# Optimization experiments

Measured on AMD Instinct MI355X. Metric: run time of the kernel, lower is better.

Reference implementation:

```python
import jax, jax.numpy as jnp
import numpy as np

DIM = 1024
NUM_HEADS = 16
HEAD_DIM = DIM // NUM_HEADS  # 64
WINDOW = 256
SCALE = HEAD_DIM ** -0.5


def setup_inputs() -> dict:
    key = jax.random.key(0)
    ks = jax.random.split(key, 5)
    B, L = 4, 4096
    x = jax.random.normal(ks[0], (B, L, DIM), dtype=jnp.float32)
    # Linear weights stored torch-style as (out_features, in_features)
    q_w = jax.random.normal(ks[1], (DIM, DIM), dtype=jnp.float32) * (DIM ** -0.5)
    kv_w = jax.random.normal(ks[2], (2 * HEAD_DIM, DIM), dtype=jnp.float32) * (DIM ** -0.5)
    proj_w = jax.random.normal(ks[3], (DIM, DIM), dtype=jnp.float32) * (DIM ** -0.5)
    proj_b = jax.random.normal(ks[4], (DIM,), dtype=jnp.float32) * 0.01
    return {"x": x, "q_w": q_w, "kv_w": kv_w, "proj_w": proj_w, "proj_b": proj_b}


def reference(x, q_w, kv_w, proj_w, proj_b):
    B, L, D = x.shape
    H, hd, ws = NUM_HEADS, HEAD_DIM, WINDOW
    # MQA projections
    q = x @ q_w.T                                  # (B, L, D)
    kv = x @ kv_w.T                                # (B, L, 2*hd)
    k, v = kv[..., :hd], kv[..., hd:]              # (B, L, hd) single KV head
    q = q.reshape(B, L, H, hd).transpose(0, 2, 1, 3)  # (B, H, L, hd)
    # Pad sequence to a multiple of the window size (static at trace time)
    pad = (ws - L % ws) % ws
    Lp = L + pad
    if pad > 0:
        q = jnp.pad(q, ((0, 0), (0, 0), (0, pad), (0, 0)))
        k = jnp.pad(k, ((0, 0), (0, pad), (0, 0)))
        v = jnp.pad(v, ((0, 0), (0, pad), (0, 0)))
    n = Lp // ws
    qb = q.reshape(B, H, n, ws, hd)                # (B, H, n, w, d)
    kb = k.reshape(B, n, ws, hd)                   # (B, n, w, d) broadcast over heads
    vb = v.reshape(B, n, ws, hd)
    # Dense per-window attention with MQA-aware KV broadcast (no expand)
    attn = jnp.einsum('bhnwd,bnud->bhnwu', qb, kb) * SCALE
    attn = jax.nn.softmax(attn, axis=-1)
    out = jnp.einsum('bhnwu,bnud->bhnwd', attn, vb)  # (B, H, n, w, d)
    out = out.reshape(B, H, Lp, hd)[:, :, :L, :]
    out = out.transpose(0, 2, 1, 3).reshape(B, L, D)  # b h l d -> b l (h d)
    return out @ proj_w.T + proj_b
```

## Files before the change

kernel.cpp:

```cpp
#include <hip/hip_runtime.h>

typedef short bf16x8 __attribute__((ext_vector_type(8)));
typedef float f32x4 __attribute__((ext_vector_type(4)));

#define QSCALE 0.18033688011112042f

__device__ __forceinline__ unsigned short f2bf(float x) {
  unsigned int u = __float_as_uint(x);
  u = (u + 0x7FFFu + ((u >> 16) & 1u)) >> 16;
  return (unsigned short)u;
}

__device__ __forceinline__ unsigned pack_rn(float a, float b) {
  unsigned au = __float_as_uint(a) + 0x8000u;
  unsigned bu = __float_as_uint(b) + 0x8000u;
  return (bu & 0xFFFF0000u) | (au >> 16);
}

__device__ __forceinline__ void async16(const void* g, void* l) {
  typedef const __attribute__((address_space(1))) unsigned int* gp_t;
  typedef __attribute__((address_space(3))) unsigned int* lp_t;
  __builtin_amdgcn_global_load_lds((gp_t)g, (lp_t)l, 16, 0, 0);
}

union frag_u { bf16x8 f; unsigned int u[4]; };

__global__ void cast_bf16(const float* __restrict__ in, unsigned short* __restrict__ out, int n4) {
  int i = blockIdx.x * 256 + threadIdx.x;
  if (i >= n4) return;
  float4 v = ((const float4*)in)[i];
  ushort4 o;
  o.x = f2bf(v.x); o.y = f2bf(v.y); o.z = f2bf(v.z); o.w = f2bf(v.w);
  ((ushort4*)out)[i] = o;
}

__global__ void cast_w3(const float* __restrict__ qw, const float* __restrict__ kvw,
                        const float* __restrict__ pw, unsigned short* __restrict__ qwo,
                        unsigned short* __restrict__ kvwo, unsigned short* __restrict__ pwo) {
  int i = blockIdx.x * 256 + threadIdx.x;
  const float* src; unsigned short* dst; int j;
  if (i < 262144)      { src = qw;  dst = qwo;  j = i; }
  else if (i < 294912) { src = kvw; dst = kvwo; j = i - 262144; }
  else                 { src = pw;  dst = pwo;  j = i - 294912; }
  float4 v = ((const float4*)src)[j];
  ushort4 o;
  o.x = f2bf(v.x); o.y = f2bf(v.y); o.z = f2bf(v.z); o.w = f2bf(v.w);
  ((ushort4*)dst)[j] = o;
}

template<int MODE>
__global__ __launch_bounds__(512, 2) void gemm256(
    const unsigned short* __restrict__ A,
    const unsigned short* __restrict__ Bw,
    unsigned short* __restrict__ Cbf,
    float* __restrict__ Cf,
    const float* __restrict__ bias,
    const float oscale,
    int M, int N, int K)
{
  __shared__ unsigned short S[65536];
  const int t = threadIdx.x;
  const int lane = t & 63, wave = t >> 6;
  const int g = lane >> 4, r = lane & 15;
  const int wm = wave >> 2, wn = wave & 3;

  const int nby = N >> 8;
  const int cpx = gridDim.x >> 3;
  const int bid = blockIdx.x;
  const int swz = (bid & 7) * cpx + (bid >> 3);
  const long row0 = (long)(swz / nby) * 256;
  const long col0 = (long)(swz % nby) * 256;

  const int NT = K >> 6;

  auto stage = [&](const unsigned short* gsrc, long grow0, int kcol0, int region) {
#pragma unroll
    for (int i = 0; i < 2; ++i) {
      int o = (i * 512 + t) << 4;
      int row = o >> 7;
      int scol = (o & 127) ^ ((row & 7) << 4);
      async16(gsrc + (grow0 + row) * K + kcol0 + (scol >> 1),
              (char*)S + region + i * 8192 + wave * 1024);
    }
  };
  auto ldA = [&](int bo, int ar, int ks) {
    return *(const bf16x8*)((const char*)S + bo + ar * 128 +
                            ((ks * 64 + g * 16) ^ ((ar & 7) << 4)));
  };
  auto ldB = [&](int bo, int br, int ks) {
    return *(const bf16x8*)((const char*)S + bo + 32768 + br * 128 +
                            ((ks * 64 + g * 16) ^ ((br & 7) << 4)));
  };

  f32x4 acc[8][4] = {};
  bf16x8 aF[4][2], b01[2][2], b23[2][2];

  stage(A,  row0,       0, 0);
  stage(A,  row0 + 128, 0, 16384);
  stage(Bw, col0,       0, 32768);
  stage(Bw, col0 + 128, 0, 32768 + 16384);
  if (NT > 1) {
    stage(Bw, col0,       64, 65536 + 32768);
    stage(Bw, col0 + 128, 64, 65536 + 32768 + 16384);
    asm volatile("s_waitcnt vmcnt(4)" ::: "memory");
  } else {
    asm volatile("s_waitcnt vmcnt(0)" ::: "memory");
  }
  __builtin_amdgcn_s_barrier();

  for (int kt = 0; kt < NT; ++kt) {
    const int bo = (kt & 1) << 16;
#pragma unroll
    for (int mf = 0; mf < 4; ++mf) {
      int ar = wm * 128 + mf * 16 + r;
      aF[mf][0] = ldA(bo, ar, 0); aF[mf][1] = ldA(bo, ar, 1);
    }
#pragma unroll
    for (int nf = 0; nf < 2; ++nf) {
      int br = wn * 64 + nf * 16 + r;
      b01[nf][0] = ldB(bo, br, 0); b01[nf][1] = ldB(bo, br, 1);
    }
    if (kt + 1 < NT) stage(A, row0, (kt + 1) * 64, bo ^ 65536);
    __builtin_amdgcn_s_barrier();
    __builtin_amdgcn_s_setprio(1);
#pragma unroll
    for (int mf = 0; mf < 4; ++mf)
#pragma unroll
      for (int nf = 0; nf < 2; ++nf) {
        acc[mf][nf] = __builtin_amdgcn_mfma_f32_16x16x32_bf16(aF[mf][0], b01[nf][0], acc[mf][nf], 0, 0, 0);
        acc[mf][nf] = __builtin_amdgcn_mfma_f32_16x16x32_bf16(aF[mf][1], b01[nf][1], acc[mf][nf], 0, 0, 0);
      }
    __builtin_amdgcn_s_setprio(0);
#pragma unroll
    for (int nf = 0; nf < 2; ++nf) {
      int br = wn * 64 + (nf + 2) * 16 + r;
      b23[nf][0] = ldB(bo, br, 0); b23[nf][1] = ldB(bo, br, 1);
    }
    if (kt + 1 < NT) stage(A, row0 + 128, (kt + 1) * 64, (bo ^ 65536) + 16384);
    __builtin_amdgcn_s_barrier();
    __builtin_amdgcn_s_setprio(1);
#pragma unroll
    for (int mf = 0; mf < 4; ++mf)
#pragma unroll
      for (int nf = 0; nf < 2; ++nf) {
        acc[mf][nf + 2] = __builtin_amdgcn_mfma_f32_16x16x32_bf16(aF[mf][0], b23[nf][0], acc[mf][nf + 2], 0, 0, 0);
        acc[mf][nf + 2] = __builtin_amdgcn_mfma_f32_16x16x32_bf16(aF[mf][1], b23[nf][1], acc[mf][nf + 2], 0, 0, 0);
      }
    __builtin_amdgcn_s_setprio(0);
#pragma unroll
    for (int mf = 0; mf < 4; ++mf) {
      int ar = wm * 128 + (mf + 4) * 16 + r;
      aF[mf][0] = ldA(bo, ar, 0); aF[mf][1] = ldA(bo, ar, 1);
    }
    if (kt + 2 < NT) stage(Bw, col0, (kt + 2) * 64, bo + 32768);
    __builtin_amdgcn_s_barrier();
    __builtin_amdgcn_s_setprio(1);
#pragma unroll
    for (int mf = 0; mf < 4; ++mf)
#pragma unroll
      for (int nf = 0; nf < 2; ++nf) {
        acc[mf + 4][nf + 2] = __builtin_amdgcn_mfma_f32_16x16x32_bf16(aF[mf][0], b23[nf][0], acc[mf + 4][nf + 2], 0, 0, 0);
        acc[mf + 4][nf + 2] = __builtin_amdgcn_mfma_f32_16x16x32_bf16(aF[mf][1], b23[nf][1], acc[mf + 4][nf + 2], 0, 0, 0);
      }
    __builtin_amdgcn_s_setprio(0);
    if (kt + 2 < NT) stage(Bw, col0 + 128, (kt + 2) * 64, bo + 32768 + 16384);
    __builtin_amdgcn_s_setprio(1);
#pragma unroll
    for (int mf = 0; mf < 4; ++mf)
#pragma unroll
      for (int nf = 0; nf < 2; ++nf) {
        acc[mf + 4][nf] = __builtin_amdgcn_mfma_f32_16x16x32_bf16(aF[mf][0], b01[nf][0], acc[mf + 4][nf], 0, 0, 0);
        acc[mf + 4][nf] = __builtin_amdgcn_mfma_f32_16x16x32_bf16(aF[mf][1], b01[nf][1], acc[mf + 4][nf], 0, 0, 0);
      }
    __builtin_amdgcn_s_setprio(0);
    if (kt < NT - 2)      asm volatile("s_waitcnt vmcnt(4)" ::: "memory");
    else if (kt < NT - 1) asm volatile("s_waitcnt vmcnt(0)" ::: "memory");
    if (kt < NT - 1) __builtin_amdgcn_s_barrier();
  }

  if (MODE == 0) {
#pragma unroll
    for (int mf = 0; mf < 8; ++mf)
#pragma unroll
      for (int nf = 0; nf < 4; ++nf) {
        long rr = row0 + wm * 128 + mf * 16 + g * 4;
        long cc = col0 + wn * 64 + nf * 16 + r;
#pragma unroll
        for (int i = 0; i < 4; ++i)
          Cbf[(rr + i) * N + cc] = f2bf(acc[mf][nf][i] * oscale);
      }
  } else {
#pragma unroll
    for (int mf = 0; mf < 8; ++mf)
#pragma unroll
      for (int nf = 0; nf < 4; ++nf) {
        long rr = row0 + wm * 128 + mf * 16 + g * 4;
        long cc = col0 + wn * 64 + nf * 16 + r;
        float bb = bias[cc];
#pragma unroll
        for (int i = 0; i < 4; ++i)
          Cf[(rr + i) * N + cc] = acc[mf][nf][i] + bb;
      }
  }
}

__global__ __launch_bounds__(256) void gemm_kv(
    const unsigned short* __restrict__ A,
    const unsigned short* __restrict__ Bw,
    unsigned short* __restrict__ Kout,
    unsigned short* __restrict__ VTout,
    int M, int N, int K)
{
  __shared__ unsigned short As[128 * 64];
  __shared__ unsigned short Bs[128 * 64];
  const int t = threadIdx.x;
  const int lane = t & 63, wave = t >> 6;
  const int g = lane >> 4, r = lane & 15;
  const int wr = wave >> 1, wc = wave & 1;
  const long row0 = (long)blockIdx.x * 128;
  const long col0 = 0;

  f32x4 acc[4][4] = {};

  for (int kt = 0; kt < K; kt += 64) {
    __syncthreads();
#pragma unroll
    for (int i = 0; i < 4; ++i) {
      int o = (i * 256 + t) << 4;
      int arow = o >> 7;
      int scol = (o & 127) ^ ((arow & 7) << 4);
      async16(A + (row0 + arow) * K + kt + (scol >> 1), (char*)As + (i * 4096 + wave * 1024));
    }
#pragma unroll
    for (int i = 0; i < 4; ++i) {
      int o = (i * 256 + t) << 4;
      int brow = o >> 7;
      int scol = (o & 127) ^ ((brow & 7) << 4);
      async16(Bw + (col0 + brow) * K + kt + (scol >> 1), (char*)Bs + (i * 4096 + wave * 1024));
    }
    __syncthreads();
#pragma unroll
    for (int ks = 0; ks < 2; ++ks) {
      bf16x8 af[4], bfr[4];
#pragma unroll
      for (int rf = 0; rf < 4; ++rf) {
        int ar = wr * 64 + rf * 16 + r;
        af[rf] = *(const bf16x8*)((const char*)As + ar * 128 + ((ks * 64 + g * 16) ^ ((ar & 7) << 4)));
      }
#pragma unroll
      for (int cf = 0; cf < 4; ++cf) {
        int br = wc * 64 + cf * 16 + r;
        bfr[cf] = *(const bf16x8*)((const char*)Bs + br * 128 + ((ks * 64 + g * 16) ^ ((br & 7) << 4)));
      }
#pragma unroll
      for (int rf = 0; rf < 4; ++rf)
#pragma unroll
        for (int cf = 0; cf < 4; ++cf)
          acc[rf][cf] = __builtin_amdgcn_mfma_f32_16x16x32_bf16(af[rf], bfr[cf], acc[rf][cf], 0, 0, 0);
    }
  }

  if (wc == 0) {
#pragma unroll
    for (int rf = 0; rf < 4; ++rf)
#pragma unroll
      for (int cf = 0; cf < 4; ++cf) {
        long rr = row0 + wr * 64 + rf * 16 + g * 4;
        int cc = cf * 16 + r;
#pragma unroll
        for (int i = 0; i < 4; ++i)
          Kout[(rr + i) * 64 + cc] = f2bf(acc[rf][cf][i]);
      }
  } else {
#pragma unroll
    for (int rf = 0; rf < 4; ++rf)
#pragma unroll
      for (int cf = 0; cf < 4; ++cf) {
        long tok = row0 + wr * 64 + rf * 16 + g * 4;
        long w16 = tok >> 8;
        int kp = (int)(tok & 255);
        int hd = cf * 16 + r;
        ushort4 pk;
        pk.x = f2bf(acc[rf][cf][0]); pk.y = f2bf(acc[rf][cf][1]);
        pk.z = f2bf(acc[rf][cf][2]); pk.w = f2bf(acc[rf][cf][3]);
        *(ushort4*)(VTout + (w16 * 64 + hd) * 256 + kp) = pk;
      }
  }
}

__global__ __launch_bounds__(512, 2) void attn_win(
    const unsigned short* __restrict__ qb,
    const unsigned short* __restrict__ kb,
    const unsigned short* __restrict__ vt,
    unsigned short* __restrict__ ao)
{
  __shared__ unsigned short Ks[256 * 64];
  __shared__ unsigned short Vs[64 * 256];

  const int blk = blockIdx.x;
  const int hp = blk & 7;
  const int w16 = blk >> 3;
  const long tok0 = (long)w16 * 256;
  const int t = threadIdx.x;
  const int lane = t & 63, wave = t >> 6;
  const int g = lane >> 4, r = lane & 15;
  const int h = hp * 2 + (wave >> 2);
  const int qw = wave & 3;

#pragma unroll
  for (int i = 0; i < 4; ++i) {
    int o = (i * 512 + t) << 4;
    int row = o >> 7;
    int ph = ((row & 3) << 1) | ((row >> 3) & 1);
    int scol = (o & 127) ^ (ph << 4);
    async16(kb + (tok0 + row) * 64 + (scol >> 1), (char*)Ks + i * 8192 + wave * 1024);
  }
  const unsigned short* vbase = vt + (long)w16 * (64 * 256);
#pragma unroll
  for (int i = 0; i < 4; ++i) {
    int o = (i * 512 + t) << 4;
    int hd = o >> 9;
    int scol = (o & 511) ^ ((hd & 7) << 4);
    async16(vbase + (long)hd * 256 + (scol >> 1), (char*)Vs + i * 8192 + wave * 1024);
  }

  bf16x8 qf[4][2];
#pragma unroll
  for (int cq = 0; cq < 4; ++cq)
#pragma unroll
    for (int kh = 0; kh < 2; ++kh)
      qf[cq][kh] = *(const bf16x8*)(qb + (tok0 + qw * 64 + cq * 16 + r) * 1024 + h * 64 + kh * 32 + g * 8);

  f32x4 O[4][4] = {};
  float sp[4] = {0.f, 0.f, 0.f, 0.f};
  const int rsub = 8 * (r >> 2) + (r & 3);
  __syncthreads();

#pragma unroll
  for (int kc = 0; kc < 8; ++kc) {
    f32x4 sc[2][4] = {};
#pragma unroll
    for (int kr = 0; kr < 2; ++kr) {
      int kp = kc * 32 + kr * 4 + rsub;
      int ph = ((kp & 3) << 1) | ((kp >> 3) & 1);
      bf16x8 kf0 = *(const bf16x8*)((const char*)Ks + kp * 128 + ((g * 16) ^ (ph << 4)));
      bf16x8 kf1 = *(const bf16x8*)((const char*)Ks + kp * 128 + ((64 + g * 16) ^ (ph << 4)));
#pragma unroll
      for (int cq = 0; cq < 4; ++cq) {
        sc[kr][cq] = __builtin_amdgcn_mfma_f32_16x16x32_bf16(kf0, qf[cq][0], sc[kr][cq], 0, 0, 0);
        sc[kr][cq] = __builtin_amdgcn_mfma_f32_16x16x32_bf16(kf1, qf[cq][1], sc[kr][cq], 0, 0, 0);
      }
    }
    bf16x8 vf[4];
#pragma unroll
    for (int ch = 0; ch < 4; ++ch) {
      int hd = ch * 16 + r;
      vf[ch] = *(const bf16x8*)((const char*)Vs + hd * 512 + ((kc * 64 + g * 16) ^ ((hd & 7) << 4)));
    }
#pragma unroll
    for (int cq = 0; cq < 4; ++cq) {
#pragma unroll
      for (int kr = 0; kr < 2; ++kr)
#pragma unroll
        for (int i = 0; i < 4; ++i)
          sc[kr][cq][i] = __builtin_amdgcn_exp2f(sc[kr][cq][i]);
      sp[cq] += ((sc[0][cq][0] + sc[0][cq][1]) + (sc[0][cq][2] + sc[0][cq][3])) +
                ((sc[1][cq][0] + sc[1][cq][1]) + (sc[1][cq][2] + sc[1][cq][3]));
    }
#pragma unroll
    for (int rq = 0; rq < 4; ++rq) {
      frag_u pa;
      pa.u[0] = pack_rn(sc[0][rq][0], sc[0][rq][1]);
      pa.u[1] = pack_rn(sc[0][rq][2], sc[0][rq][3]);
      pa.u[2] = pack_rn(sc[1][rq][0], sc[1][rq][1]);
      pa.u[3] = pack_rn(sc[1][rq][2], sc[1][rq][3]);
#pragma unroll
      for (int ch = 0; ch < 4; ++ch)
        O[rq][ch] = __builtin_amdgcn_mfma_f32_16x16x32_bf16(pa.f, vf[ch], O[rq][ch], 0, 0, 0);
    }
  }
  float inv[4];
#pragma unroll
  for (int cq = 0; cq < 4; ++cq) {
    float s = sp[cq];
    s += __shfl_xor(s, 16);
    s += __shfl_xor(s, 32);
    inv[cq] = 1.0f / s;
  }
#pragma unroll
  for (int rq = 0; rq < 4; ++rq)
#pragma unroll
    for (int i = 0; i < 4; ++i) {
      float w = __shfl(inv[rq], g * 4 + i);
      long tokr = tok0 + qw * 64 + rq * 16 + g * 4 + i;
#pragma unroll
      for (int ch = 0; ch < 4; ++ch)
        ao[tokr * 1024 + h * 64 + ch * 16 + r] = f2bf(O[rq][ch][i] * w);
    }
}

extern "C" void kernel_launch(void* const* d_in, const int* in_sizes, int n_in,
                              void* d_out, int out_size, void* d_ws, size_t ws_size,
                              hipStream_t stream) {
  const float* x      = (const float*)d_in[0];
  const float* q_w    = (const float*)d_in[1];
  const float* kv_w   = (const float*)d_in[2];
  const float* proj_w = (const float*)d_in[3];
  const float* proj_b = (const float*)d_in[4];

  char* ws = (char*)d_ws;
  unsigned short* x_bf   = (unsigned short*)(ws + 0);
  unsigned short* q_bf   = (unsigned short*)(ws + 33554432);
  unsigned short* ao_bf  = (unsigned short*)(ws + 67108864);
  unsigned short* qw_bf  = (unsigned short*)(ws + 100663296);
  unsigned short* pw_bf  = (unsigned short*)(ws + 102760448);
  unsigned short* kvw_bf = (unsigned short*)(ws + 104857600);
  unsigned short* k_bf   = (unsigned short*)(ws + 105119744);
  unsigned short* vt_bf  = (unsigned short*)(ws + 107216896);
  if (ws_size < 109314048) return;

  cast_bf16<<<16384, 256, 0, stream>>>(x, x_bf, 4194304);
  cast_w3<<<2176, 256, 0, stream>>>(q_w, kv_w, proj_w, qw_bf, kvw_bf, pw_bf);

  gemm256<0><<<256, 512, 0, stream>>>(x_bf, qw_bf, q_bf, nullptr, nullptr, QSCALE, 16384, 1024, 1024);
  gemm_kv<<<128, 256, 0, stream>>>(x_bf, kvw_bf, k_bf, vt_bf, 16384, 128, 1024);
  attn_win<<<512, 512, 0, stream>>>(q_bf, k_bf, vt_bf, ao_bf);
  gemm256<1><<<256, 512, 0, stream>>>(ao_bf, pw_bf, nullptr, (float*)d_out, proj_b, 1.0f, 16384, 1024, 1024);
}
```

Baseline: 148.2 us.

## Fuse x fp32-to-bf16 cast into the KV projection GEMM

Removes the standalone cast_bf16 kernel and has the KV projection GEMM read x in fp32, convert it to bf16 in registers, write it to LDS for the MFMA, and also store the bf16 copy to global for the later Q GEMM. The KV GEMM now runs before the Q GEMM with 64-row tiles and 256 blocks, which saves one full read of x and one kernel launch. In exchange, the A-tile load becomes synchronous register loads instead of async LDS loads. Rounding also changes from round-to-nearest-even to pack_rn's simpler round-half-up, which alters bf16 values slightly.

```diff
diff --git a/kernel.cpp b/kernel.cpp
--- a/kernel.cpp
+++ b/kernel.cpp
@@ -2,6 +2,7 @@
 
 typedef short bf16x8 __attribute__((ext_vector_type(8)));
 typedef float f32x4 __attribute__((ext_vector_type(4)));
+typedef unsigned int u32x4 __attribute__((ext_vector_type(4)));
 
 #define QSCALE 0.18033688011112042f
 
@@ -24,15 +25,6 @@
 }
 
 union frag_u { bf16x8 f; unsigned int u[4]; };
-
-__global__ void cast_bf16(const float* __restrict__ in, unsigned short* __restrict__ out, int n4) {
-  int i = blockIdx.x * 256 + threadIdx.x;
-  if (i >= n4) return;
-  float4 v = ((const float4*)in)[i];
-  ushort4 o;
-  o.x = f2bf(v.x); o.y = f2bf(v.y); o.z = f2bf(v.z); o.w = f2bf(v.w);
-  ((ushort4*)out)[i] = o;
-}
 
 __global__ void cast_w3(const float* __restrict__ qw, const float* __restrict__ kvw,
                         const float* __restrict__ pw, unsigned short* __restrict__ qwo,
@@ -204,47 +196,57 @@
   }
 }
 
-__global__ __launch_bounds__(256) void gemm_kv(
-    const unsigned short* __restrict__ A,
+__global__ __launch_bounds__(256) void gemm_kv_cast(
+    const float* __restrict__ x,
     const unsigned short* __restrict__ Bw,
+    unsigned short* __restrict__ xbf,
     unsigned short* __restrict__ Kout,
-    unsigned short* __restrict__ VTout,
-    int M, int N, int K)
+    unsigned short* __restrict__ VTout)
 {
-  __shared__ unsigned short As[128 * 64];
+  __shared__ unsigned short As[64 * 64];
   __shared__ unsigned short Bs[128 * 64];
   const int t = threadIdx.x;
   const int lane = t & 63, wave = t >> 6;
   const int g = lane >> 4, r = lane & 15;
   const int wr = wave >> 1, wc = wave & 1;
-  const long row0 = (long)blockIdx.x * 128;
-  const long col0 = 0;
-
-  f32x4 acc[4][4] = {};
-
-  for (int kt = 0; kt < K; kt += 64) {
+  const long row0 = (long)blockIdx.x * 64;
+  const int arow = t >> 2, aq = t & 3;
+
+  f32x4 acc[2][4] = {};
+
+  for (int kt = 0; kt < 1024; kt += 64) {
     __syncthreads();
-#pragma unroll
-    for (int i = 0; i < 4; ++i) {
-      int o = (i * 256 + t) << 4;
-      int arow = o >> 7;
-      int scol = (o & 127) ^ ((arow & 7) << 4);
-      async16(A + (row0 + arow) * K + kt + (scol >> 1), (char*)As + (i * 4096 + wave * 1024));
-    }
+    float4 av[4];
+    const float4* src = (const float4*)(x + (row0 + arow) * 1024 + kt + aq * 16);
+#pragma unroll
+    for (int i = 0; i < 4; ++i) av[i] = src[i];
 #pragma unroll
     for (int i = 0; i < 4; ++i) {
       int o = (i * 256 + t) << 4;
       int brow = o >> 7;
       int scol = (o & 127) ^ ((brow & 7) << 4);
-      async16(Bw + (col0 + brow) * K + kt + (scol >> 1), (char*)Bs + (i * 4096 + wave * 1024));
+      async16(Bw + brow * 1024 + kt + (scol >> 1), (char*)Bs + i * 4096 + wave * 1024);
+    }
+    u32x4 u0, u1;
+    u0[0] = pack_rn(av[0].x, av[0].y); u0[1] = pack_rn(av[0].z, av[0].w);
+    u0[2] = pack_rn(av[1].x, av[1].y); u0[3] = pack_rn(av[1].z, av[1].w);
+    u1[0] = pack_rn(av[2].x, av[2].y); u1[1] = pack_rn(av[2].z, av[2].w);
+    u1[2] = pack_rn(av[3].x, av[3].y); u1[3] = pack_rn(av[3].z, av[3].w);
+    {
+      char* base = (char*)As + arow * 128;
+      *(u32x4*)(base + ((aq * 32) ^ ((arow & 7) << 4))) = u0;
+      *(u32x4*)(base + ((aq * 32 + 16) ^ ((arow & 7) << 4))) = u1;
+      char* gb = (char*)(xbf + (row0 + arow) * 1024 + kt + aq * 16);
+      *(u32x4*)(gb) = u0;
+      *(u32x4*)(gb + 16) = u1;
     }
     __syncthreads();
 #pragma unroll
     for (int ks = 0; ks < 2; ++ks) {
-      bf16x8 af[4], bfr[4];
-#pragma unroll
-      for (int rf = 0; rf < 4; ++rf) {
-        int ar = wr * 64 + rf * 16 + r;
+      bf16x8 af[2], bfr[4];
+#pragma unroll
+      for (int rf = 0; rf < 2; ++rf) {
+        int ar = wr * 32 + rf * 16 + r;
         af[rf] = *(const bf16x8*)((const char*)As + ar * 128 + ((ks * 64 + g * 16) ^ ((ar & 7) << 4)));
       }
 #pragma unroll
@@ -253,7 +255,7 @@
         bfr[cf] = *(const bf16x8*)((const char*)Bs + br * 128 + ((ks * 64 + g * 16) ^ ((br & 7) << 4)));
       }
 #pragma unroll
-      for (int rf = 0; rf < 4; ++rf)
+      for (int rf = 0; rf < 2; ++rf)
 #pragma unroll
         for (int cf = 0; cf < 4; ++cf)
           acc[rf][cf] = __builtin_amdgcn_mfma_f32_16x16x32_bf16(af[rf], bfr[cf], acc[rf][cf], 0, 0, 0);
@@ -262,10 +264,10 @@
 
   if (wc == 0) {
 #pragma unroll
-    for (int rf = 0; rf < 4; ++rf)
+    for (int rf = 0; rf < 2; ++rf)
 #pragma unroll
       for (int cf = 0; cf < 4; ++cf) {
-        long rr = row0 + wr * 64 + rf * 16 + g * 4;
+        long rr = row0 + wr * 32 + rf * 16 + g * 4;
         int cc = cf * 16 + r;
 #pragma unroll
         for (int i = 0; i < 4; ++i)
@@ -273,10 +275,10 @@
       }
   } else {
 #pragma unroll
-    for (int rf = 0; rf < 4; ++rf)
+    for (int rf = 0; rf < 2; ++rf)
 #pragma unroll
       for (int cf = 0; cf < 4; ++cf) {
-        long tok = row0 + wr * 64 + rf * 16 + g * 4;
+        long tok = row0 + wr * 32 + rf * 16 + g * 4;
         long w16 = tok >> 8;
         int kp = (int)(tok & 255);
         int hd = cf * 16 + r;
@@ -419,11 +421,10 @@
   unsigned short* vt_bf  = (unsigned short*)(ws + 107216896);
   if (ws_size < 109314048) return;
 
-  cast_bf16<<<16384, 256, 0, stream>>>(x, x_bf, 4194304);
   cast_w3<<<2176, 256, 0, stream>>>(q_w, kv_w, proj_w, qw_bf, kvw_bf, pw_bf);
+  gemm_kv_cast<<<256, 256, 0, stream>>>(x, kvw_bf, x_bf, k_bf, vt_bf);
 
   gemm256<0><<<256, 512, 0, stream>>>(x_bf, qw_bf, q_bf, nullptr, nullptr, QSCALE, 16384, 1024, 1024);
-  gemm_kv<<<128, 256, 0, stream>>>(x_bf, kvw_bf, k_bf, vt_bf, 16384, 128, 1024);
   attn_win<<<512, 512, 0, stream>>>(q_bf, k_bf, vt_bf, ao_bf);
   gemm256<1><<<256, 512, 0, stream>>>(ao_bf, pw_bf, nullptr, (float*)d_out, proj_b, 1.0f, 16384, 1024, 1024);
 }
```

Measured after the change: 142.8 us. 3.6% less time.
